# Performance work log

Measured on AMD Instinct MI355X. Metric: run time of the kernel, lower is better.

The kernel has to match this reference:

```python
import jax, jax.numpy as jnp
import numpy as np

H = 4          # num attention heads
C1 = 64        # channel_num[0]
C2 = 128       # channel_num[1]
KV = C1 + C2   # 192
MLP = C1 * 4   # expand_ratio=4


def _layernorm(x, g, b, eps=1e-6):
    m = jnp.mean(x, axis=-1, keepdims=True)
    v = jnp.mean((x - m) ** 2, axis=-1, keepdims=True)
    return (x - m) * jax.lax.rsqrt(v + eps) * g + b


def setup_inputs() -> dict:
    key = jax.random.key(0)
    ks = jax.random.split(key, 12)
    B, N = 8, 3136
    s_q = 1.0 / np.sqrt(C1)
    s_kv = 1.0 / np.sqrt(KV)
    return {
        "emb1": jax.random.normal(ks[0], (B, N, C1), jnp.float32),
        "emb2": jax.random.normal(ks[1], (B, N, C2), jnp.float32),
        # per-head projection weights (nn.Linear convention: y = x @ W.T)
        "Wq": jax.random.uniform(ks[2], (H, C1, C1), jnp.float32, -s_q, s_q),
        "Wk": jax.random.uniform(ks[3], (H, KV, KV), jnp.float32, -s_kv, s_kv),
        "Wv": jax.random.uniform(ks[4], (H, KV, KV), jnp.float32, -s_kv, s_kv),
        "Wout": jax.random.uniform(ks[5], (C1, C1), jnp.float32, -s_q, s_q),
        "ln1_g": jnp.ones((C1,), jnp.float32),
        "ln1_b": jnp.zeros((C1,), jnp.float32),
        "lnall_g": jnp.ones((KV,), jnp.float32),
        "lnall_b": jnp.zeros((KV,), jnp.float32),
        "ffn_g": jnp.ones((C1,), jnp.float32),
        "ffn_b": jnp.zeros((C1,), jnp.float32),
        "fc1_w": jax.random.uniform(ks[6], (MLP, C1), jnp.float32, -s_q, s_q),
        "fc1_b": jnp.zeros((MLP,), jnp.float32),
        "fc2_w": jax.random.uniform(ks[7], (C1, MLP), jnp.float32, -1.0 / np.sqrt(MLP), 1.0 / np.sqrt(MLP)),
        "fc2_b": jnp.zeros((C1,), jnp.float32),
    }


def reference(emb1, emb2, Wq, Wk, Wv, Wout, ln1_g, ln1_b, lnall_g, lnall_b,
              ffn_g, ffn_b, fc1_w, fc1_b, fc2_w, fc2_b):
    # emb1: [B,N,C1], emb2: [B,N,C2]
    emb_all = jnp.concatenate([emb1, emb2], axis=2)          # [B,N,KV]
    cx1 = _layernorm(emb1, ln1_g, ln1_b)                     # [B,N,C1]
    ea = _layernorm(emb_all, lnall_g, lnall_b)               # [B,N,KV]

    # batched per-head projections (replaces Python loop over ModuleList)
    qT = jnp.einsum('bnc,hdc->bhdn', cx1, Wq)                # [B,H,C1,N]
    k = jnp.einsum('bnk,hdk->bhnd', ea, Wk)                  # [B,H,N,KV]
    vT = jnp.einsum('bnk,hdk->bhdn', ea, Wv)                 # [B,H,KV,N]

    scores = jnp.einsum('bhcn,bhnk->bhck', qT, k) / np.sqrt(KV)  # [B,H,C1,KV]
    # InstanceNorm2d over spatial dims (C1, KV) per (batch, head), affine=False
    m = jnp.mean(scores, axis=(2, 3), keepdims=True)
    v = jnp.mean((scores - m) ** 2, axis=(2, 3), keepdims=True)
    scores = (scores - m) * jax.lax.rsqrt(v + 1e-5)
    probs = jax.nn.softmax(scores, axis=3)                   # softmax over KV

    ctx = jnp.einsum('bhck,bhkn->bhcn', probs, vT)           # [B,H,C1,N]
    ctx = jnp.mean(ctx, axis=1).transpose(0, 2, 1)           # mean over heads -> [B,N,C1]
    o = ctx @ Wout.T                                         # [B,N,C1]

    cx = emb1 + o                                            # residual
    x = _layernorm(cx, ffn_g, ffn_b)
    x = jax.nn.gelu(x @ fc1_w.T + fc1_b, approximate=False)
    x = x @ fc2_w.T + fc2_b
    return x + cx
```

## Files before the change

kernel.cpp:

```cpp
#include <hip/hip_runtime.h>
#include <hip/hip_bf16.h>

typedef __hip_bfloat16 bf;
typedef unsigned short ushort_t;
typedef __attribute__((ext_vector_type(8))) short short8;
typedef __attribute__((ext_vector_type(4))) float f32x4;

#define NB 8
#define SEQ 3136
#define HD 4

__device__ __forceinline__ float lo_bf(unsigned u){ return __uint_as_float(u << 16); }
__device__ __forceinline__ float hi_bf(unsigned u){ return __uint_as_float(u & 0xffff0000u); }
__device__ __forceinline__ float b16f(ushort_t s){ return __uint_as_float(((unsigned)s) << 16); }
__device__ __forceinline__ unsigned short f2bfbits(float f){
  unsigned u = __float_as_uint(f);
  unsigned r = u + 0x7fffu + ((u >> 16) & 1u);
  return (unsigned short)(r >> 16);
}
__device__ __forceinline__ float ldin(const void* p, long i, bool isbf){
  return isbf ? __bfloat162float(((const bf*)p)[i]) : ((const float*)p)[i];
}
__device__ __forceinline__ ushort_t cvt1(const void* p, long i, bool isbf){
  return isbf ? ((const ushort_t*)p)[i] : f2bfbits(((const float*)p)[i]);
}
#define DTYPE_FLAG(p) (((const unsigned*)(p))[0] == 0x3F803F80u)

__device__ __forceinline__ float wsum(float v){
  #pragma unroll
  for (int o = 32; o > 0; o >>= 1) v += __shfl_xor(v, o, 64);
  return v;
}
__device__ __forceinline__ float wmax(float v){
  #pragma unroll
  for (int o = 32; o > 0; o >>= 1) v = fmaxf(v, __shfl_xor(v, o, 64));
  return v;
}

__global__ __launch_bounds__(256) void k_g(
    const void* __restrict__ emb1, const void* __restrict__ emb2,
    const void* __restrict__ g1, const void* __restrict__ b1,
    const void* __restrict__ ga, const void* __restrict__ ba,
    const void* __restrict__ Wq, const void* __restrict__ Wk, const void* __restrict__ Wv,
    const void* __restrict__ f1w, const void* __restrict__ f2w, const void* __restrict__ Wout,
    ushort_t* __restrict__ part, ushort_t* __restrict__ eag,
    ushort_t* __restrict__ Wqb, ushort_t* __restrict__ Wkb, ushort_t* __restrict__ WvTb,
    ushort_t* __restrict__ f1wb, ushort_t* __restrict__ f2wb,
    ushort_t* __restrict__ Woutb, unsigned* __restrict__ cnt){
  bool isbf = DTYPE_FLAG(g1);
  int tid = threadIdx.x;
  int b = blockIdx.y, ch = blockIdx.x;
  if (ch >= 49){
    if (b != 0) return;
    int g = (ch - 49)*256 + tid;
    const int STR = 24*256;
    if (g < 8) cnt[g] = 0;
    for (int i = g; i < 16384; i += STR) Wqb[i] = cvt1(Wq, i, isbf);
    for (int i = g; i < 4096;  i += STR) Woutb[i] = cvt1(Wout, i, isbf);
    for (int i = g; i < 147456; i += STR) Wkb[i] = cvt1(Wk, i, isbf);
    for (int i = g; i < 147456; i += STR){
      int hh = i / 36864, r = i - hh*36864;
      int j = r / 192, e = r - j*192;
      WvTb[i] = cvt1(Wv, (long)hh*36864 + e*192 + j, isbf);
    }
    for (int i = g; i < 16384; i += STR) f1wb[i] = cvt1(f1w, i, isbf);
    for (int i = g; i < 16384; i += STR) f2wb[i] = cvt1(f2w, i, isbf);
    return;
  }
  __shared__ __align__(16) ushort_t z1t[64*72];
  __shared__ __align__(16) ushort_t zat[192*72];
  int wave = tid >> 6, lane = tid & 63;
  int quad = lane >> 4, nl = lane & 15;
  long t0 = (long)b*SEQ + ch*64;
  float g1l = ldin(g1,lane,isbf), b1l = ldin(b1,lane,isbf);
  float ga0 = ldin(ga,lane,isbf),     ba0 = ldin(ba,lane,isbf);
  float ga1 = ldin(ga,64+lane,isbf),  ba1 = ldin(ba,64+lane,isbf);
  float ga2 = ldin(ga,128+lane,isbf), ba2 = ldin(ba,128+lane,isbf);
  #pragma unroll 4
  for (int k = 0; k < 16; ++k){
    int tok = wave*16 + k;
    long t = t0 + tok;
    float e1  = ldin(emb1, t*64 + lane, isbf);
    float e2a = ldin(emb2, t*128 + lane, isbf);
    float e2b = ldin(emb2, t*128 + 64 + lane, isbf);
    float s1 = wsum(e1), ss1 = wsum(e1*e1);
    float m1 = s1*(1.f/64.f);
    float r1 = rsqrtf(fmaxf(ss1*(1.f/64.f) - m1*m1, 0.f) + 1e-6f);
    z1t[lane*72 + tok] = f2bfbits((e1 - m1)*r1*g1l + b1l);
    float s23 = wsum(e2a+e2b), ss23 = wsum(e2a*e2a + e2b*e2b);
    float ma = (s1+s23)*(1.f/192.f);
    float ra = rsqrtf(fmaxf((ss1+ss23)*(1.f/192.f) - ma*ma, 0.f) + 1e-6f);
    unsigned short za0 = f2bfbits((e1  - ma)*ra*ga0 + ba0);
    unsigned short za1 = f2bfbits((e2a - ma)*ra*ga1 + ba1);
    unsigned short za2 = f2bfbits((e2b - ma)*ra*ga2 + ba2);
    zat[lane*72 + tok]       = za0;
    zat[(64+lane)*72 + tok]  = za1;
    zat[(128+lane)*72 + tok] = za2;
    eag[t*192 + lane]       = za0;
    eag[t*192 + 64 + lane]  = za1;
    eag[t*192 + 128 + lane] = za2;
  }
  __syncthreads();
  short8 a0 = *reinterpret_cast<const short8*>(&z1t[(wave*16+nl)*72 + quad*8]);
  short8 a1 = *reinterpret_cast<const short8*>(&z1t[(wave*16+nl)*72 + 32 + quad*8]);
  ushort_t* P = part + ((long)b*49 + ch)*12288;
  #pragma unroll
  for (int nt = 0; nt < 12; ++nt){
    f32x4 cd = {0.f,0.f,0.f,0.f};
    short8 b0 = *reinterpret_cast<const short8*>(&zat[(nt*16+nl)*72 + quad*8]);
    cd = __builtin_amdgcn_mfma_f32_16x16x32_bf16(a0, b0, cd, 0, 0, 0);
    short8 b1v = *reinterpret_cast<const short8*>(&zat[(nt*16+nl)*72 + 32 + quad*8]);
    cd = __builtin_amdgcn_mfma_f32_16x16x32_bf16(a1, b1v, cd, 0, 0, 0);
    #pragma unroll
    for (int reg = 0; reg < 4; ++reg)
      P[(wave*16 + quad*4 + reg)*192 + nt*16 + nl] = f2bfbits(cd[reg]);
  }
}

__global__ __launch_bounds__(64) void k_red(
    const ushort_t* __restrict__ part, ushort_t* __restrict__ Gb){
  int idx4 = blockIdx.x*64 + threadIdx.x;
  int b = idx4 / 3072, e4 = idx4 - b*3072;
  const ushort_t* p = part + (long)b*49*12288 + e4*4;
  float s0=0.f, s1=0.f, s2=0.f, s3=0.f;
  #pragma unroll
  for (int ch = 0; ch < 49; ++ch){
    uint2 u = *reinterpret_cast<const uint2*>(p + (long)ch*12288);
    s0 += lo_bf(u.x); s1 += hi_bf(u.x); s2 += lo_bf(u.y); s3 += hi_bf(u.y);
  }
  unsigned lo = (unsigned)f2bfbits(s0) | ((unsigned)f2bfbits(s1) << 16);
  unsigned hi = (unsigned)f2bfbits(s2) | ((unsigned)f2bfbits(s3) << 16);
  *reinterpret_cast<uint2*>(Gb + (long)idx4*4) = make_uint2(lo, hi);
}

__global__ __launch_bounds__(256) void k_att(
    const ushort_t* __restrict__ Gb, const ushort_t* __restrict__ Wqb,
    const ushort_t* __restrict__ Wkb, const ushort_t* __restrict__ WvTb,
    const ushort_t* __restrict__ Woutb,
    float* __restrict__ Mh, unsigned* __restrict__ cnt, ushort_t* __restrict__ W2){
  __shared__ __align__(16) ushort_t sT[192*72];
  __shared__ __align__(16) float    sS[64*196];
  __shared__ __align__(16) ushort_t sPh[64*200];
  __shared__ __align__(16) ushort_t sPl[64*200];
  __shared__ float red[8];
  __shared__ float stat[2];
  __shared__ unsigned sOld;
  int h = blockIdx.x, b = blockIdx.y, z = blockIdx.z;
  int tid = threadIdx.x, wave = tid >> 6, lane = tid & 63;
  int quad = lane >> 4, nl = lane & 15;

  const ushort_t* Gp = Gb + (long)b*12288;
  short8 aG[6];
  #pragma unroll
  for (int ks = 0; ks < 6; ++ks)
    aG[ks] = *reinterpret_cast<const short8*>(Gp + (wave*16+nl)*192 + ks*32 + quad*8);
  const ushort_t* Wkp = Wkb + (long)h*36864;
  #pragma unroll
  for (int nt = 0; nt < 12; ++nt){
    f32x4 cd = {0.f,0.f,0.f,0.f};
    #pragma unroll
    for (int ks = 0; ks < 6; ++ks){
      short8 bw = *reinterpret_cast<const short8*>(Wkp + (nt*16+nl)*192 + ks*32 + quad*8);
      cd = __builtin_amdgcn_mfma_f32_16x16x32_bf16(aG[ks], bw, cd, 0, 0, 0);
    }
    #pragma unroll
    for (int reg = 0; reg < 4; ++reg)
      sT[(nt*16+nl)*72 + wave*16 + quad*4 + reg] = f2bfbits(cd[reg]);
  }
  __syncthreads();

  const ushort_t* Wqp = Wqb + (long)h*4096;
  short8 aQ[2];
  #pragma unroll
  for (int ks = 0; ks < 2; ++ks)
    aQ[ks] = *reinterpret_cast<const short8*>(Wqp + (wave*16+nl)*64 + ks*32 + quad*8);
  const float scale = 0.07216878364870323f;
  float ps = 0.f, pss = 0.f;
  #pragma unroll
  for (int nt = 0; nt < 12; ++nt){
    f32x4 cd = {0.f,0.f,0.f,0.f};
    #pragma unroll
    for (int ks = 0; ks < 2; ++ks){
      short8 bt = *reinterpret_cast<const short8*>(&sT[(nt*16+nl)*72 + ks*32 + quad*8]);
      cd = __builtin_amdgcn_mfma_f32_16x16x32_bf16(aQ[ks], bt, cd, 0, 0, 0);
    }
    #pragma unroll
    for (int reg = 0; reg < 4; ++reg){
      float v = cd[reg]*scale;
      sS[(wave*16 + quad*4 + reg)*196 + nt*16 + nl] = v;
      ps += v; pss += v*v;
    }
  }
  ps = wsum(ps); pss = wsum(pss);
  if (lane == 0){ red[wave] = ps; red[4+wave] = pss; }
  __syncthreads();
  if (tid == 0){
    float s  = red[0]+red[1]+red[2]+red[3];
    float s2 = red[4]+red[5]+red[6]+red[7];
    float m = s * (1.f/12288.f);
    stat[0] = m;
    stat[1] = rsqrtf(fmaxf(s2*(1.f/12288.f) - m*m, 0.f) + 1e-5f);
  }
  __syncthreads();
  float m = stat[0], r = stat[1];
  #pragma unroll 2
  for (int rr = 0; rr < 16; ++rr){
    int row = wave*16 + rr;
    float v0 = (sS[row*196+lane]     - m)*r;
    float v1 = (sS[row*196+64+lane]  - m)*r;
    float v2 = (sS[row*196+128+lane] - m)*r;
    float mx = wmax(fmaxf(v0, fmaxf(v1, v2)));
    float e0 = __expf(v0-mx), e1 = __expf(v1-mx), e2 = __expf(v2-mx);
    float inv = 1.f / wsum(e0+e1+e2);
    e0 *= inv; e1 *= inv; e2 *= inv;
    ushort_t h0 = f2bfbits(e0), h1 = f2bfbits(e1), h2 = f2bfbits(e2);
    sPh[row*200+lane]     = h0;  sPl[row*200+lane]     = f2bfbits(e0 - b16f(h0));
    sPh[row*200+64+lane]  = h1;  sPl[row*200+64+lane]  = f2bfbits(e1 - b16f(h1));
    sPh[row*200+128+lane] = h2;  sPl[row*200+128+lane] = f2bfbits(e2 - b16f(h2));
  }
  __syncthreads();

  short8 aPh[6], aPl[6];
  #pragma unroll
  for (int ks = 0; ks < 6; ++ks){
    aPh[ks] = *reinterpret_cast<const short8*>(&sPh[(wave*16+nl)*200 + ks*32 + quad*8]);
    aPl[ks] = *reinterpret_cast<const short8*>(&sPl[(wave*16+nl)*200 + ks*32 + quad*8]);
  }
  const ushort_t* Wvp = WvTb + (long)h*36864;
  float* Mb = Mh + ((long)b*HD + h)*12288;
  #pragma unroll
  for (int ntl = 0; ntl < 6; ++ntl){
    int nt = z*6 + ntl;
    f32x4 cdh = {0.f,0.f,0.f,0.f};
    f32x4 cdl = {0.f,0.f,0.f,0.f};
    #pragma unroll
    for (int ks = 0; ks < 6; ++ks){
      short8 bw = *reinterpret_cast<const short8*>(Wvp + (nt*16+nl)*192 + ks*32 + quad*8);
      cdl = __builtin_amdgcn_mfma_f32_16x16x32_bf16(aPl[ks], bw, cdl, 0, 0, 0);
      cdh = __builtin_amdgcn_mfma_f32_16x16x32_bf16(aPh[ks], bw, cdh, 0, 0, 0);
    }
    #pragma unroll
    for (int reg = 0; reg < 4; ++reg)
      Mb[(wave*16 + quad*4 + reg)*192 + nt*16 + nl] = cdh[reg] + cdl[reg];
  }

  __threadfence();
  if (tid == 0) sOld = atomicAdd(&cnt[b], 1u);
  __syncthreads();
  if (sOld == 7u){
    __threadfence();
    const float* M0 = Mh + (long)b*HD*12288;
    for (int g = tid; g < 3072; g += 256){
      float4 x0 = ((const float4*)M0)[g];
      float4 x1 = ((const float4*)(M0 + 12288))[g];
      float4 x2 = ((const float4*)(M0 + 24576))[g];
      float4 x3 = ((const float4*)(M0 + 36864))[g];
      int e = g*4; int c = e/192, j = e - c*192;
      sT[(j+0)*72 + c] = f2bfbits(0.25f*(x0.x+x1.x+x2.x+x3.x));
      sT[(j+1)*72 + c] = f2bfbits(0.25f*(x0.y+x1.y+x2.y+x3.y));
      sT[(j+2)*72 + c] = f2bfbits(0.25f*(x0.z+x1.z+x2.z+x3.z));
      sT[(j+3)*72 + c] = f2bfbits(0.25f*(x0.w+x1.w+x2.w+x3.w));
    }
    __syncthreads();
    short8 aW[2];
    #pragma unroll
    for (int ks = 0; ks < 2; ++ks)
      aW[ks] = *reinterpret_cast<const short8*>(Woutb + (wave*16+nl)*64 + ks*32 + quad*8);
    ushort_t* W2b = W2 + (long)b*12288;
    #pragma unroll
    for (int nt = 0; nt < 12; ++nt){
      f32x4 cd = {0.f,0.f,0.f,0.f};
      #pragma unroll
      for (int ks = 0; ks < 2; ++ks){
        short8 bm = *reinterpret_cast<const short8*>(&sT[(nt*16+nl)*72 + ks*32 + quad*8]);
        cd = __builtin_amdgcn_mfma_f32_16x16x32_bf16(aW[ks], bm, cd, 0, 0, 0);
      }
      #pragma unroll
      for (int reg = 0; reg < 4; ++reg)
        W2b[(wave*16 + quad*4 + reg)*192 + nt*16 + nl] = f2bfbits(cd[reg]);
    }
  }
}

__global__ __launch_bounds__(256) void k_tail(
    const void* __restrict__ emb1, const ushort_t* __restrict__ eag,
    const ushort_t* __restrict__ W2g,
    const void* __restrict__ ffg, const void* __restrict__ ffb,
    const ushort_t* __restrict__ f1wb, const void* __restrict__ f1b,
    const ushort_t* __restrict__ f2wb, const void* __restrict__ f2b,
    const void* __restrict__ lng, void* __restrict__ out){
  bool isbf = DTYPE_FLAG(lng);
  __shared__ __align__(16) ushort_t sCX[16*72];
  __shared__ __align__(16) ushort_t sX[16*88];
  __shared__ __align__(16) ushort_t sH[16*280];
  int tid = threadIdx.x, wave = tid >> 6, lane = tid & 63;
  int quad = lane >> 4, nl = lane & 15;
  int b = blockIdx.y;
  long tbase = (long)b*SEQ + blockIdx.x*16;

  short8 aO[6];
  #pragma unroll
  for (int kt = 0; kt < 6; ++kt)
    aO[kt] = *reinterpret_cast<const short8*>(eag + (tbase + nl)*192 + kt*32 + quad*8);
  const ushort_t* W2b = W2g + (long)b*12288;
  {
    f32x4 cd = {0.f,0.f,0.f,0.f};
    #pragma unroll
    for (int kt = 0; kt < 6; ++kt){
      short8 bf8 = *reinterpret_cast<const short8*>(W2b + (wave*16+nl)*192 + kt*32 + quad*8);
      cd = __builtin_amdgcn_mfma_f32_16x16x32_bf16(aO[kt], bf8, cd, 0, 0, 0);
    }
    #pragma unroll
    for (int reg = 0; reg < 4; ++reg){
      int tokl = quad*4 + reg;
      int chn = wave*16 + nl;
      float e1v = ldin(emb1, (tbase + tokl)*64 + chn, isbf);
      sCX[tokl*72 + chn] = f2bfbits(cd[reg] + e1v);
    }
  }
  __syncthreads();

  float gl = ldin(ffg, lane, isbf), bl = ldin(ffb, lane, isbf);
  #pragma unroll
  for (int k = 0; k < 4; ++k){
    int tokl = wave*4 + k;
    float c = b16f(sCX[tokl*72 + lane]);
    float s = wsum(c), ss = wsum(c*c);
    float m = s*(1.f/64.f);
    float r = rsqrtf(fmaxf(ss*(1.f/64.f) - m*m, 0.f) + 1e-6f);
    sX[tokl*88 + lane] = f2bfbits((c - m)*r*gl + bl);
  }
  __syncthreads();

  short8 aX[2];
  #pragma unroll
  for (int kt = 0; kt < 2; ++kt)
    aX[kt] = *reinterpret_cast<const short8*>(&sX[nl*88 + kt*32 + quad*8]);
  #pragma unroll
  for (int nn = 0; nn < 4; ++nn){
    int nt = wave*4 + nn;
    f32x4 cd = {0.f,0.f,0.f,0.f};
    #pragma unroll
    for (int kt = 0; kt < 2; ++kt){
      short8 bf8 = *reinterpret_cast<const short8*>(f1wb + (long)(nt*16+nl)*64 + kt*32 + quad*8);
      cd = __builtin_amdgcn_mfma_f32_16x16x32_bf16(aX[kt], bf8, cd, 0, 0, 0);
    }
    float bb = ldin(f1b, nt*16+nl, isbf);
    #pragma unroll
    for (int reg = 0; reg < 4; ++reg){
      float v = cd[reg] + bb;
      float h = 0.5f*v*(1.f + erff(v*0.70710678118654752f));
      sH[(quad*4 + reg)*280 + nt*16 + nl] = f2bfbits(h);
    }
  }
  __syncthreads();

  short8 aH[8];
  #pragma unroll
  for (int kt = 0; kt < 8; ++kt)
    aH[kt] = *reinterpret_cast<const short8*>(&sH[nl*280 + kt*32 + quad*8]);
  {
    f32x4 cd = {0.f,0.f,0.f,0.f};
    #pragma unroll
    for (int kt = 0; kt < 8; ++kt){
      short8 bf8 = *reinterpret_cast<const short8*>(f2wb + (long)(wave*16+nl)*256 + kt*32 + quad*8);
      cd = __builtin_amdgcn_mfma_f32_16x16x32_bf16(aH[kt], bf8, cd, 0, 0, 0);
    }
    float bb2 = ldin(f2b, wave*16+nl, isbf);
    #pragma unroll
    for (int reg = 0; reg < 4; ++reg){
      int tokl = quad*4 + reg;
      int chn = wave*16 + nl;
      float y = cd[reg] + bb2 + b16f(sCX[tokl*72 + chn]);
      if (isbf) sCX[tokl*72 + chn] = f2bfbits(y);
      else ((float*)out)[(tbase + tokl)*64 + chn] = y;
    }
  }
  if (isbf){
    __syncthreads();
    int tokl = wave*4 + (lane >> 4), prt = lane & 15;
    uint2 v = *reinterpret_cast<const uint2*>(&sCX[tokl*72 + prt*4]);
    *reinterpret_cast<uint2*>((ushort_t*)out + (tbase + tokl)*64 + prt*4) = v;
  }
}

extern "C" void kernel_launch(void* const* d_in, const int* in_sizes, int n_in,
                              void* d_out, int out_size, void* d_ws, size_t ws_size,
                              hipStream_t stream){
  const void* emb1 = d_in[0];
  const void* emb2 = d_in[1];
  const void* Wq   = d_in[2];
  const void* Wk   = d_in[3];
  const void* Wv   = d_in[4];
  const void* Wout = d_in[5];
  const void* ln1g = d_in[6];
  const void* ln1b = d_in[7];
  const void* lag  = d_in[8];
  const void* lab  = d_in[9];
  const void* ffg  = d_in[10];
  const void* ffb  = d_in[11];
  const void* f1w  = d_in[12];
  const void* f1b  = d_in[13];
  const void* f2w  = d_in[14];
  const void* f2b  = d_in[15];

  char* base = (char*)d_ws;
  ushort_t* part = (ushort_t*)base;
  ushort_t* ea   = (ushort_t*)(base + 9633792);
  ushort_t* Gb   = (ushort_t*)(base + 19267584);
  float*    Mh   = (float*)(base + 19464192);
  ushort_t* W2   = (ushort_t*)(base + 21037056);
  ushort_t* Wqb  = (ushort_t*)(base + 21233664);
  ushort_t* Wkb  = (ushort_t*)(base + 21266432);
  ushort_t* WvTb = (ushort_t*)(base + 21561344);
  ushort_t* f1wb = (ushort_t*)(base + 21856256);
  ushort_t* f2wb = (ushort_t*)(base + 21889024);
  ushort_t* Woutb= (ushort_t*)(base + 21921792);
  unsigned* cnt  = (unsigned*)(base + 21929984);

  k_g   <<<dim3(73,NB),    256, 0, stream>>>(emb1, emb2, ln1g, ln1b, lag, lab,
                                             Wq, Wk, Wv, f1w, f2w, Wout,
                                             part, ea, Wqb, Wkb, WvTb, f1wb, f2wb,
                                             Woutb, cnt);
  k_red <<<384,             64, 0, stream>>>(part, Gb);
  k_att <<<dim3(HD,NB,2),  256, 0, stream>>>(Gb, Wqb, Wkb, WvTb, Woutb, Mh, cnt, W2);
  k_tail<<<dim3(196,NB),   256, 0, stream>>>(emb1, ea, W2, ffg, ffb,
                                             f1wb, f1b, f2wb, f2b, ln1g, d_out);
}
```

Before: 181.3 us.

## Split attention kernel across more z-blocks, keep scores in registers, prefetch weights

The attention kernel grid grows from 2 to 6 z-slices, so each block computes 2 output column tiles of the V projection instead of 6, raising parallelism across the tiny grid. Scores now stay in registers and softmax is done with 16-lane shuffles, which removes the shared-memory score buffer and its round trip. Wk tiles are double-buffered in registers and the Wv tiles are preloaded before the softmax to hide load latency. The trade-off is that each z-block redundantly recomputes the K projection and scores, and register pressure rises.

After: 182.9 us. About the same (+0.9%).

```diff
diff --git a/kernel.cpp b/kernel.cpp
--- a/kernel.cpp
+++ b/kernel.cpp
@@ -9,6 +9,7 @@
 #define NB 8
 #define SEQ 3136
 #define HD 4
+#define ZS 6
 
 __device__ __forceinline__ float lo_bf(unsigned u){ return __uint_as_float(u << 16); }
 __device__ __forceinline__ float hi_bf(unsigned u){ return __uint_as_float(u & 0xffff0000u); }
@@ -29,11 +30,6 @@
 __device__ __forceinline__ float wsum(float v){
   #pragma unroll
   for (int o = 32; o > 0; o >>= 1) v += __shfl_xor(v, o, 64);
-  return v;
-}
-__device__ __forceinline__ float wmax(float v){
-  #pragma unroll
-  for (int o = 32; o > 0; o >>= 1) v = fmaxf(v, __shfl_xor(v, o, 64));
   return v;
 }
 
@@ -139,7 +135,6 @@
     const ushort_t* __restrict__ Woutb,
     float* __restrict__ Mh, unsigned* __restrict__ cnt, ushort_t* __restrict__ W2){
   __shared__ __align__(16) ushort_t sT[192*72];
-  __shared__ __align__(16) float    sS[64*196];
   __shared__ __align__(16) ushort_t sPh[64*200];
   __shared__ __align__(16) ushort_t sPl[64*200];
   __shared__ float red[8];
@@ -155,17 +150,26 @@
   for (int ks = 0; ks < 6; ++ks)
     aG[ks] = *reinterpret_cast<const short8*>(Gp + (wave*16+nl)*192 + ks*32 + quad*8);
   const ushort_t* Wkp = Wkb + (long)h*36864;
+  short8 bcur[6], bnxt[6];
+  #pragma unroll
+  for (int ks = 0; ks < 6; ++ks)
+    bcur[ks] = *reinterpret_cast<const short8*>(Wkp + (long)nl*192 + ks*32 + quad*8);
   #pragma unroll
   for (int nt = 0; nt < 12; ++nt){
-    f32x4 cd = {0.f,0.f,0.f,0.f};
-    #pragma unroll
-    for (int ks = 0; ks < 6; ++ks){
-      short8 bw = *reinterpret_cast<const short8*>(Wkp + (nt*16+nl)*192 + ks*32 + quad*8);
-      cd = __builtin_amdgcn_mfma_f32_16x16x32_bf16(aG[ks], bw, cd, 0, 0, 0);
-    }
+    if (nt < 11){
+      #pragma unroll
+      for (int ks = 0; ks < 6; ++ks)
+        bnxt[ks] = *reinterpret_cast<const short8*>(Wkp + (long)((nt+1)*16+nl)*192 + ks*32 + quad*8);
+    }
+    f32x4 cd = {0.f,0.f,0.f,0.f};
+    #pragma unroll
+    for (int ks = 0; ks < 6; ++ks)
+      cd = __builtin_amdgcn_mfma_f32_16x16x32_bf16(aG[ks], bcur[ks], cd, 0, 0, 0);
     #pragma unroll
     for (int reg = 0; reg < 4; ++reg)
       sT[(nt*16+nl)*72 + wave*16 + quad*4 + reg] = f2bfbits(cd[reg]);
+    #pragma unroll
+    for (int ks = 0; ks < 6; ++ks) bcur[ks] = bnxt[ks];
   }
   __syncthreads();
 
@@ -175,6 +179,7 @@
   for (int ks = 0; ks < 2; ++ks)
     aQ[ks] = *reinterpret_cast<const short8*>(Wqp + (wave*16+nl)*64 + ks*32 + quad*8);
   const float scale = 0.07216878364870323f;
+  float sv[12][4];
   float ps = 0.f, pss = 0.f;
   #pragma unroll
   for (int nt = 0; nt < 12; ++nt){
@@ -187,7 +192,7 @@
     #pragma unroll
     for (int reg = 0; reg < 4; ++reg){
       float v = cd[reg]*scale;
-      sS[(wave*16 + quad*4 + reg)*196 + nt*16 + nl] = v;
+      sv[nt][reg] = v;
       ps += v; pss += v*v;
     }
   }
@@ -202,21 +207,45 @@
     stat[1] = rsqrtf(fmaxf(s2*(1.f/12288.f) - m*m, 0.f) + 1e-5f);
   }
   __syncthreads();
+
+  const ushort_t* Wvp = WvTb + (long)h*36864;
+  short8 bv[2][6];
+  #pragma unroll
+  for (int ntl = 0; ntl < 2; ++ntl)
+    #pragma unroll
+    for (int ks = 0; ks < 6; ++ks)
+      bv[ntl][ks] = *reinterpret_cast<const short8*>(Wvp + (long)((z*2+ntl)*16+nl)*192 + ks*32 + quad*8);
+
   float m = stat[0], r = stat[1];
-  #pragma unroll 2
-  for (int rr = 0; rr < 16; ++rr){
-    int row = wave*16 + rr;
-    float v0 = (sS[row*196+lane]     - m)*r;
-    float v1 = (sS[row*196+64+lane]  - m)*r;
-    float v2 = (sS[row*196+128+lane] - m)*r;
-    float mx = wmax(fmaxf(v0, fmaxf(v1, v2)));
-    float e0 = __expf(v0-mx), e1 = __expf(v1-mx), e2 = __expf(v2-mx);
-    float inv = 1.f / wsum(e0+e1+e2);
-    e0 *= inv; e1 *= inv; e2 *= inv;
-    ushort_t h0 = f2bfbits(e0), h1 = f2bfbits(e1), h2 = f2bfbits(e2);
-    sPh[row*200+lane]     = h0;  sPl[row*200+lane]     = f2bfbits(e0 - b16f(h0));
-    sPh[row*200+64+lane]  = h1;  sPl[row*200+64+lane]  = f2bfbits(e1 - b16f(h1));
-    sPh[row*200+128+lane] = h2;  sPl[row*200+128+lane] = f2bfbits(e2 - b16f(h2));
+  #pragma unroll
+  for (int reg = 0; reg < 4; ++reg){
+    float mx = -3.4e38f;
+    #pragma unroll
+    for (int nt = 0; nt < 12; ++nt){
+      float v = (sv[nt][reg] - m)*r;
+      sv[nt][reg] = v;
+      mx = fmaxf(mx, v);
+    }
+    #pragma unroll
+    for (int o = 1; o < 16; o <<= 1) mx = fmaxf(mx, __shfl_xor(mx, o, 64));
+    float sum = 0.f;
+    #pragma unroll
+    for (int nt = 0; nt < 12; ++nt){
+      float e = __expf(sv[nt][reg] - mx);
+      sv[nt][reg] = e;
+      sum += e;
+    }
+    #pragma unroll
+    for (int o = 1; o < 16; o <<= 1) sum += __shfl_xor(sum, o, 64);
+    float inv = 1.f / sum;
+    int row = wave*16 + quad*4 + reg;
+    #pragma unroll
+    for (int nt = 0; nt < 12; ++nt){
+      float e = sv[nt][reg]*inv;
+      ushort_t hi = f2bfbits(e);
+      sPh[row*200 + nt*16 + nl] = hi;
+      sPl[row*200 + nt*16 + nl] = f2bfbits(e - b16f(hi));
+    }
   }
   __syncthreads();
 
@@ -226,18 +255,16 @@
     aPh[ks] = *reinterpret_cast<const short8*>(&sPh[(wave*16+nl)*200 + ks*32 + quad*8]);
     aPl[ks] = *reinterpret_cast<const short8*>(&sPl[(wave*16+nl)*200 + ks*32 + quad*8]);
   }
-  const ushort_t* Wvp = WvTb + (long)h*36864;
   float* Mb = Mh + ((long)b*HD + h)*12288;
   #pragma unroll
-  for (int ntl = 0; ntl < 6; ++ntl){
-    int nt = z*6 + ntl;
+  for (int ntl = 0; ntl < 2; ++ntl){
+    int nt = z*2 + ntl;
     f32x4 cdh = {0.f,0.f,0.f,0.f};
     f32x4 cdl = {0.f,0.f,0.f,0.f};
     #pragma unroll
     for (int ks = 0; ks < 6; ++ks){
-      short8 bw = *reinterpret_cast<const short8*>(Wvp + (nt*16+nl)*192 + ks*32 + quad*8);
-      cdl = __builtin_amdgcn_mfma_f32_16x16x32_bf16(aPl[ks], bw, cdl, 0, 0, 0);
-      cdh = __builtin_amdgcn_mfma_f32_16x16x32_bf16(aPh[ks], bw, cdh, 0, 0, 0);
+      cdl = __builtin_amdgcn_mfma_f32_16x16x32_bf16(aPl[ks], bv[ntl][ks], cdl, 0, 0, 0);
+      cdh = __builtin_amdgcn_mfma_f32_16x16x32_bf16(aPh[ks], bv[ntl][ks], cdh, 0, 0, 0);
     }
     #pragma unroll
     for (int reg = 0; reg < 4; ++reg)
@@ -247,7 +274,7 @@
   __threadfence();
   if (tid == 0) sOld = atomicAdd(&cnt[b], 1u);
   __syncthreads();
-  if (sOld == 7u){
+  if (sOld == HD*ZS - 1u){
     __threadfence();
     const float* M0 = Mh + (long)b*HD*12288;
     for (int g = tid; g < 3072; g += 256){
@@ -418,12 +445,12 @@
   ushort_t* Woutb= (ushort_t*)(base + 21921792);
   unsigned* cnt  = (unsigned*)(base + 21929984);
 
-  k_g   <<<dim3(73,NB),    256, 0, stream>>>(emb1, emb2, ln1g, ln1b, lag, lab,
-                                             Wq, Wk, Wv, f1w, f2w, Wout,
-                                             part, ea, Wqb, Wkb, WvTb, f1wb, f2wb,
-                                             Woutb, cnt);
-  k_red <<<384,             64, 0, stream>>>(part, Gb);
-  k_att <<<dim3(HD,NB,2),  256, 0, stream>>>(Gb, Wqb, Wkb, WvTb, Woutb, Mh, cnt, W2);
-  k_tail<<<dim3(196,NB),   256, 0, stream>>>(emb1, ea, W2, ffg, ffb,
-                                             f1wb, f1b, f2wb, f2b, ln1g, d_out);
-}
+  k_g   <<<dim3(73,NB),     256, 0, stream>>>(emb1, emb2, ln1g, ln1b, lag, lab,
+                                              Wq, Wk, Wv, f1w, f2w, Wout,
+                                              part, ea, Wqb, Wkb, WvTb, f1wb, f2wb,
+                                              Woutb, cnt);
+  k_red <<<384,              64, 0, stream>>>(part, Gb);
+  k_att <<<dim3(HD,NB,ZS),  256, 0, stream>>>(Gb, Wqb, Wkb, WvTb, Woutb, Mh, cnt, W2);
+  k_tail<<<dim3(196,NB),    256, 0, stream>>>(emb1, ea, W2, ffg, ffb,
+                                              f1wb, f1b, f2wb, f2b, ln1g, d_out);
+}
```
